# Kernel optimization log

Measured on AMD Instinct MI355X. Metric: run time of the kernel, lower is better.

Reference implementation:

```python
import jax, jax.numpy as jnp
import numpy as np

COMMITMENT_COST = 0.25


def l2norm(x, eps=1e-12):
    # F.normalize along last dim
    n = jnp.linalg.norm(x, axis=-1, keepdims=True)
    return x / jnp.maximum(n, eps)


def vector_quantize(x, codebook, commitment_cost):
    """Euclidean VQ: cdist + argmin, straight-through, VQ loss + perplexity.
    x: (B, N, D), codebook: (K, D)."""
    B, N, D = x.shape
    K = codebook.shape[0]
    flat = x.reshape(-1, D)  # (BN, D)
    # squared euclidean distances via expansion (no (BN,K,D) intermediate)
    d = (jnp.sum(flat * flat, axis=-1, keepdims=True)
         - 2.0 * flat @ codebook.T
         + jnp.sum(codebook * codebook, axis=-1))  # (BN, K)
    idx = jnp.argmin(d, axis=-1)  # (BN,)
    q = codebook[idx]  # (BN, D)
    # VQ losses
    e_latent = jnp.mean((jax.lax.stop_gradient(q) - flat) ** 2)
    q_latent = jnp.mean((q - jax.lax.stop_gradient(flat)) ** 2)
    loss = q_latent + commitment_cost * e_latent
    # perplexity over codebook usage (bincount, not dense one-hot)
    counts = jnp.zeros((K,), flat.dtype).at[idx].add(1.0)
    probs = counts / idx.shape[0]
    perplexity = jnp.exp(-jnp.sum(probs * jnp.log(probs + 1e-10)))
    return idx.reshape(B, N), perplexity, loss


def transform_mfcc(X):
    # wave_embedding.transform_freq: normalize frames, then rfft -> real -> bins 2:40
    Xn = l2norm(X)
    spec = jnp.fft.rfft(Xn, axis=-1).real[..., 2:40]  # (B, N, 38)
    return l2norm(spec)  # mfcc_embedding.norm_fn


def setup_inputs() -> dict:
    key = jax.random.key(0)
    k1, k2, k3 = jax.random.split(key, 3)
    X = jax.random.normal(k1, (16, 4096, 80), dtype=jnp.float32)
    wave_codebook = jax.random.normal(k2, (1024, 80), dtype=jnp.float32)
    mfcc_codebook = jax.random.normal(k3, (256, 38), dtype=jnp.float32)
    return {"X": X, "wave_codebook": wave_codebook, "mfcc_codebook": mfcc_codebook}


def reference(X, wave_codebook, mfcc_codebook):
    K_wave = wave_codebook.shape[0]
    wave_idx, wave_ppl, wave_loss = vector_quantize(X, wave_codebook, COMMITMENT_COST)
    X_mfcc = transform_mfcc(X)
    mfcc_idx, mfcc_ppl, mfcc_loss = vector_quantize(X_mfcc, mfcc_codebook, COMMITMENT_COST)
    mfcc_idx = mfcc_idx + K_wave
    # rearrange stack([wave, mfcc], dim=1): 'b c n -> b (n c)' -> interleave per frame
    B, N = wave_idx.shape
    encodings = jnp.stack([wave_idx, mfcc_idx], axis=-1).reshape(B, 2 * N)
    return encodings, wave_ppl, wave_loss, mfcc_ppl, mfcc_loss
```

## Files before the change

kernel.cpp:

```cpp
#include <hip/hip_runtime.h>
#include <hip/hip_bf16.h>
#include <math.h>


#define NROWS 65536
#define DW    80
#define KW    1024
#define DM    38
#define KM    256
#define CHUNK 128
#define NCHK  8
#define CT_PER 8

typedef __attribute__((ext_vector_type(8))) short bf16x8;
typedef __attribute__((ext_vector_type(4))) float f32x4;

__device__ __forceinline__ void bf16split(float v, short& h, short& l) {
    __hip_bfloat16 hb = __float2bfloat16(v);
    float hf = __bfloat162float(hb);
    __hip_bfloat16 lb = __float2bfloat16(v - hf);
    h = *(short*)&hb;
    l = *(short*)&lb;
}

__device__ __forceinline__ void bf16split3(float v, short& a, short& b, short& c) {
    __hip_bfloat16 h = __float2bfloat16(v);
    float hf = __bfloat162float(h);
    float r = v - hf;
    __hip_bfloat16 m = __float2bfloat16(r);
    float mf = __bfloat162float(m);
    __hip_bfloat16 lo = __float2bfloat16(r - mf);
    a = *(short*)&h; b = *(short*)&m; c = *(short*)&lo;
}

__device__ __forceinline__ bf16x8 bf8zero() {
    bf16x8 z;
    #pragma unroll
    for (int j = 0; j < 8; ++j) z[j] = 0;
    return z;
}

#define WS_SUMS   0
#define WS_HIST   256
#define WS_CNW    5376
#define WS_CNM    9472
#define WS_COSTAB 10496
#define WS_CTF    23296
#define WS_CBF    46336

__global__ __launch_bounds__(256) void prep_kernel(
    const float* __restrict__ cbw, const float* __restrict__ cbm,
    float* __restrict__ sums, int* __restrict__ hist,
    float* __restrict__ cn_w, float* __restrict__ cn_m,
    float* __restrict__ costab)
{
    int idx = blockIdx.x * 256 + threadIdx.x;
    if (idx < KW) {
        const float* p = cbw + (size_t)idx * DW;
        float s = 0.f;
        for (int i = 0; i < DW; ++i) s = fmaf(p[i], p[i], s);
        cn_w[idx] = s;
    } else if (idx < KW + KM) {
        int i = idx - KW;
        const float* p = cbm + (size_t)i * DM;
        float s = 0.f;
        for (int j = 0; j < DM; ++j) s = fmaf(p[j], p[j], s);
        cn_m[i] = s;
    } else if (idx < KW + KM + DW * 40) {
        int t = idx - (KW + KM);
        int d = t / 40, j = t % 40;
        double v = (j < DM)
            ? cos(2.0 * 3.14159265358979323846 * (double)((j + 2) * d) / 80.0)
            : 0.0;
        costab[t] = (float)v;
    } else if (idx == KW + KM + DW * 40)      sums[0] = 0.f;
    else if (idx == KW + KM + DW * 40 + 1)    sums[1] = 0.f;
    else if (idx >= 4482 && idx < 4482 + 1280) hist[idx - 4482] = 0;
}

__global__ __launch_bounds__(256) void prep2_kernel(
    const float* __restrict__ costab, const float* __restrict__ cbm,
    short* __restrict__ ctf, short* __restrict__ cbf)
{
    int idx = blockIdx.x * 256 + threadIdx.x;
    if (idx < 3840) {
        int col, k;
        if (idx < 3072) {
            int j = idx & 7, l = (idx >> 3) & 63, t = idx >> 9;
            col = (t >> 1) * 16 + (l & 15);
            k = 32 * (t & 1) + 8 * (l >> 4) + j;
        } else {
            int i2 = idx - 3072;
            int j = i2 & 7, l = (i2 >> 3) & 31, ct = i2 >> 8;
            col = ct * 16 + (l & 15);
            k = 64 + 8 * (l >> 4) + j;
        }
        float v = (col < 40) ? costab[k * 40 + col] : 0.f;
        short a, b, c; bf16split3(v, a, b, c);
        ctf[idx] = a; ctf[3840 + idx] = b; ctf[7680 + idx] = c;
    } else if (idx < 16128) {
        int i3 = idx - 3840;
        int code, k;
        if (i3 < 8192) {
            int j = i3 & 7, l = (i3 >> 3) & 63, ct = i3 >> 9;
            code = ct * 16 + (l & 15);
            k = 8 * (l >> 4) + j;
        } else {
            int i4 = i3 - 8192;
            int j = i4 & 7, l = (i4 >> 3) & 31, ct = i4 >> 8;
            code = ct * 16 + (l & 15);
            k = 32 + 8 * (l >> 4) + j;
        }
        float v = (k < DM) ? cbm[(size_t)code * DM + k] : 0.f;
        short a, b, c; bf16split3(v, a, b, c);
        cbf[i3] = a; cbf[12288 + i3] = b; cbf[24576 + i3] = c;
    }
}

__global__ __launch_bounds__(256) void wave_vq_mfma(
    const float* __restrict__ X, const float* __restrict__ cb,
    const float* __restrict__ cn, float* __restrict__ out,
    float* __restrict__ sums)
{
    __shared__ short Bh[2][CT_PER * 3 * 64 * 8];
    __shared__ short Bl[2][CT_PER * 3 * 64 * 8];
    __shared__ float cnl[2][CHUNK];
    __shared__ float redw[4];

    const int tid = threadIdx.x;
    const int l   = tid & 63;
    const int qu  = tid >> 6;
    const int c16 = l & 15;
    const int g   = l >> 4;
    const size_t rowbase = (size_t)blockIdx.x * 256 + (size_t)qu * 64;

    bf16x8 Ah[4][3], Al[4][3];
    float xs2[4] = {0.f, 0.f, 0.f, 0.f};
    #pragma unroll
    for (int rt = 0; rt < 4; ++rt) {
        #pragma unroll
        for (int s = 0; s < 3; ++s) {
            const int k0 = 32 * s + 8 * g;
            bf16x8 ah, al;
            if (k0 < DW) {
                const float4* ap =
                    (const float4*)(X + (rowbase + rt * 16 + c16) * DW + k0);
                float4 u = ap[0], w = ap[1];
                float f[8] = {u.x, u.y, u.z, u.w, w.x, w.y, w.z, w.w};
                #pragma unroll
                for (int j = 0; j < 8; ++j) {
                    short hh, ll;
                    bf16split(f[j], hh, ll);
                    ah[j] = hh; al[j] = ll;
                    xs2[rt] = fmaf(f[j], f[j], xs2[rt]);
                }
            } else {
                ah = bf8zero(); al = bf8zero();
            }
            Ah[rt][s] = ah; Al[rt][s] = al;
        }
    }
    #pragma unroll
    for (int rt = 0; rt < 4; ++rt) {
        xs2[rt] += __shfl_xor(xs2[rt], 16, 64);
        xs2[rt] += __shfl_xor(xs2[rt], 32, 64);
    }

    for (int i = tid; i < CT_PER * 32 * 8; i += 256) {
        int ctt = i >> 8;
        int rem = i & 255;
        int lane = 32 + (rem >> 3), j = rem & 7;
        int off = ((ctt * 3 + 2) * 64 + lane) * 8 + j;
        Bh[0][off] = 0; Bh[1][off] = 0; Bl[0][off] = 0; Bl[1][off] = 0;
    }

    auto stage = [&](int c, int b) {
        const float4* src = (const float4*)(cb + (size_t)c * CHUNK * DW);
        #pragma unroll
        for (int i = 0; i < 10; ++i) {
            int q4 = i * 256 + tid;
            float4 v = src[q4];
            int cl = q4 / 20;
            int kb = (q4 - cl * 20) * 4;
            int ctt = cl >> 4, cc = cl & 15;
            int s = kb >> 5, kl = kb & 31, gg = kl >> 3, j0 = kl & 7;
            int off = ((ctt * 3 + s) * 64 + gg * 16 + cc) * 8 + j0;
            short h0, h1, h2, h3, l0, l1, l2, l3;
            bf16split(v.x, h0, l0); bf16split(v.y, h1, l1);
            bf16split(v.z, h2, l2); bf16split(v.w, h3, l3);
            short4 hv = {h0, h1, h2, h3}, lv = {l0, l1, l2, l3};
            *(short4*)&Bh[b][off] = hv;
            *(short4*)&Bl[b][off] = lv;
        }
        if (tid < CHUNK) cnl[b][tid] = cn[c * CHUNK + tid];
    };

    stage(0, 0);
    __syncthreads();

    float bd[4][4];
    int   bi[4][4];
    #pragma unroll
    for (int rt = 0; rt < 4; ++rt)
        #pragma unroll
        for (int i = 0; i < 4; ++i) { bd[rt][i] = 3.4e38f; bi[rt][i] = 0; }

    for (int ch = 0; ch < NCHK; ++ch) {
        const int cur = ch & 1;
        for (int ct = 0; ct < CT_PER; ++ct) {
            const float cnv = cnl[cur][ct * 16 + c16];
            f32x4 acc[4];
            #pragma unroll
            for (int rt = 0; rt < 4; ++rt) acc[rt] = (f32x4){0.f, 0.f, 0.f, 0.f};
            #pragma unroll
            for (int s = 0; s < 3; ++s) {
                const int bo = ((ct * 3 + s) * 64 + l) * 8;
                bf16x8 bh = *(const bf16x8*)&Bh[cur][bo];
                bf16x8 bl = *(const bf16x8*)&Bl[cur][bo];
                #pragma unroll
                for (int rt = 0; rt < 4; ++rt)
                    acc[rt] = __builtin_amdgcn_mfma_f32_16x16x32_bf16(Al[rt][s], bl, acc[rt], 0, 0, 0);
                #pragma unroll
                for (int rt = 0; rt < 4; ++rt)
                    acc[rt] = __builtin_amdgcn_mfma_f32_16x16x32_bf16(Ah[rt][s], bl, acc[rt], 0, 0, 0);
                #pragma unroll
                for (int rt = 0; rt < 4; ++rt)
                    acc[rt] = __builtin_amdgcn_mfma_f32_16x16x32_bf16(Al[rt][s], bh, acc[rt], 0, 0, 0);
                #pragma unroll
                for (int rt = 0; rt < 4; ++rt)
                    acc[rt] = __builtin_amdgcn_mfma_f32_16x16x32_bf16(Ah[rt][s], bh, acc[rt], 0, 0, 0);
            }
            const int idxbase = ch * CHUNK + ct * 16 + c16;
            #pragma unroll
            for (int rt = 0; rt < 4; ++rt) {
                #pragma unroll
                for (int i = 0; i < 4; ++i) {
                    float d = fmaf(-2.f, acc[rt][i], cnv);
                    if (d < bd[rt][i]) { bd[rt][i] = d; bi[rt][i] = idxbase; }
                }
            }
        }
        if (ch + 1 < NCHK) stage(ch + 1, cur ^ 1);
        __syncthreads();
    }

    float lw = 0.f;
    #pragma unroll
    for (int rt = 0; rt < 4; ++rt) {
        #pragma unroll
        for (int i = 0; i < 4; ++i) {
            float d = bd[rt][i]; int ix = bi[rt][i];
            #pragma unroll
            for (int m = 1; m < 16; m <<= 1) {
                float d2 = __shfl_xor(d, m, 64);
                int   i2 = __shfl_xor(ix, m, 64);
                if (d2 < d || (d2 == d && i2 < ix)) { d = d2; ix = i2; }
            }
            float xn = __shfl(xs2[rt], (l & 48) + 4 * (l >> 4) + i, 64);
            if (c16 == 0) {
                size_t row = rowbase + rt * 16 + 4 * g + i;
                out[2 * row] = (float)ix;
                lw += d + xn;
            }
        }
    }
    #pragma unroll
    for (int m = 1; m < 64; m <<= 1) lw += __shfl_xor(lw, m, 64);
    if (l == 0) redw[qu] = lw;
    __syncthreads();
    if (tid == 0) atomicAdd(&sums[0], redw[0] + redw[1] + redw[2] + redw[3]);
}

__global__ __launch_bounds__(256) void mfcc_mfma(
    const float* __restrict__ X, const float* __restrict__ cn_m,
    const short* __restrict__ ctf, const short* __restrict__ cbf,
    float* __restrict__ out, float* __restrict__ sums)
{
    __shared__ __align__(16) short CT2[11520];
    __shared__ __align__(16) short CB2[36864];
    __shared__ float XF[4][64 * 49];
    __shared__ float CN[KM];
    __shared__ float red4[4];

    const int tid = threadIdx.x;
    const int l   = tid & 63;
    const int w   = tid >> 6;
    const int c16 = l & 15;
    const int g   = l >> 4;
    const size_t rowbase = (size_t)blockIdx.x * 256 + (size_t)w * 64;

    {
        const int4* s1 = (const int4*)ctf;
        for (int i = tid; i < 1440; i += 256) ((int4*)CT2)[i] = s1[i];
        const int4* s2 = (const int4*)cbf;
        for (int i = tid; i < 4608; i += 256) ((int4*)CB2)[i] = s2[i];
        if (tid < KM) CN[tid] = cn_m[tid];
    }
    __syncthreads();

    float* xfl = &XF[w][0];

    #pragma unroll 1
    for (int rt = 0; rt < 4; ++rt) {
        bf16x8 A0[3], A1[3], A2[3];
        #pragma unroll
        for (int s = 0; s < 3; ++s) {
            const int k0 = 32 * s + 8 * g;
            if (k0 < DW) {
                const float4* ap =
                    (const float4*)(X + (rowbase + rt * 16 + c16) * DW + k0);
                float4 u = ap[0], v = ap[1];
                float f[8] = {u.x, u.y, u.z, u.w, v.x, v.y, v.z, v.w};
                bf16x8 a0, a1, a2;
                #pragma unroll
                for (int j = 0; j < 8; ++j) {
                    short aa, bb, cc;
                    bf16split3(f[j], aa, bb, cc);
                    a0[j] = aa; a1[j] = bb; a2[j] = cc;
                }
                A0[s] = a0; A1[s] = a1; A2[s] = a2;
            } else {
                A0[s] = bf8zero(); A1[s] = bf8zero(); A2[s] = bf8zero();
            }
        }

        f32x4 acc[3];
        #pragma unroll
        for (int ct = 0; ct < 3; ++ct) acc[ct] = (f32x4){0.f, 0.f, 0.f, 0.f};

        #pragma unroll
        for (int s = 0; s < 3; ++s) {
            #pragma unroll
            for (int ct = 0; ct < 3; ++ct) {
                bf16x8 b0, b1, b2;
                if (s < 2) {
                    const int off = ((ct * 2 + s) * 64 + l) * 8;
                    b0 = *(const bf16x8*)&CT2[off];
                    b1 = *(const bf16x8*)&CT2[3840 + off];
                    b2 = *(const bf16x8*)&CT2[7680 + off];
                } else if (l < 32) {
                    const int off = 3072 + (ct * 32 + l) * 8;
                    b0 = *(const bf16x8*)&CT2[off];
                    b1 = *(const bf16x8*)&CT2[3840 + off];
                    b2 = *(const bf16x8*)&CT2[7680 + off];
                } else {
                    b0 = bf8zero(); b1 = bf8zero(); b2 = bf8zero();
                }
                acc[ct] = __builtin_amdgcn_mfma_f32_16x16x32_bf16(A2[s], b0, acc[ct], 0, 0, 0);
                acc[ct] = __builtin_amdgcn_mfma_f32_16x16x32_bf16(A1[s], b1, acc[ct], 0, 0, 0);
                acc[ct] = __builtin_amdgcn_mfma_f32_16x16x32_bf16(A0[s], b2, acc[ct], 0, 0, 0);
                acc[ct] = __builtin_amdgcn_mfma_f32_16x16x32_bf16(A1[s], b0, acc[ct], 0, 0, 0);
                acc[ct] = __builtin_amdgcn_mfma_f32_16x16x32_bf16(A0[s], b1, acc[ct], 0, 0, 0);
                acc[ct] = __builtin_amdgcn_mfma_f32_16x16x32_bf16(A0[s], b0, acc[ct], 0, 0, 0);
            }
        }

        #pragma unroll
        for (int i = 0; i < 4; ++i) {
            float n2 = acc[0][i] * acc[0][i];
            n2 = fmaf(acc[1][i], acc[1][i], n2);
            n2 = fmaf(acc[2][i], acc[2][i], n2);
            #pragma unroll
            for (int m = 1; m < 16; m <<= 1) n2 += __shfl_xor(n2, m, 64);
            float inv = 1.0f / fmaxf(sqrtf(n2), 1e-12f);
            const int row_l = rt * 16 + 4 * g + i;
            #pragma unroll
            for (int ct = 0; ct < 3; ++ct)
                xfl[row_l * 49 + ct * 16 + c16] = acc[ct][i] * inv;
        }
    }
    __syncthreads();

    bf16x8 X0[4][3], X1[4][3];
    #pragma unroll
    for (int rt = 0; rt < 4; ++rt) {
        const int r0 = rt * 16 + c16;
        {
            const float* p = &xfl[r0 * 49 + 8 * g];
            bf16x8 q0, q1, q2;
            #pragma unroll
            for (int j = 0; j < 8; ++j) {
                short aa, bb, cc;
                bf16split3(p[j], aa, bb, cc);
                q0[j] = aa; q1[j] = bb; q2[j] = cc;
            }
            X0[rt][0] = q0; X0[rt][1] = q1; X0[rt][2] = q2;
        }
        if (g < 2) {
            const float* p = &xfl[r0 * 49 + 32 + 8 * g];
            bf16x8 q0, q1, q2;
            #pragma unroll
            for (int j = 0; j < 8; ++j) {
                short aa, bb, cc;
                bf16split3(p[j], aa, bb, cc);
                q0[j] = aa; q1[j] = bb; q2[j] = cc;
            }
            X1[rt][0] = q0; X1[rt][1] = q1; X1[rt][2] = q2;
        } else {
            X1[rt][0] = bf8zero(); X1[rt][1] = bf8zero(); X1[rt][2] = bf8zero();
        }
    }

    float bd[4][4];
    int   bi[4][4];
    #pragma unroll
    for (int rt = 0; rt < 4; ++rt)
        #pragma unroll
        for (int i = 0; i < 4; ++i) { bd[rt][i] = 3.4e38f; bi[rt][i] = 0; }

    #pragma unroll 1
    for (int ct = 0; ct < 16; ++ct) {
        bf16x8 B0[3], B1[3];
        const int off0 = (ct * 64 + l) * 8;
        B0[0] = *(const bf16x8*)&CB2[off0];
        B0[1] = *(const bf16x8*)&CB2[12288 + off0];
        B0[2] = *(const bf16x8*)&CB2[24576 + off0];
        if (l < 32) {
            const int off1 = 8192 + (ct * 32 + l) * 8;
            B1[0] = *(const bf16x8*)&CB2[off1];
            B1[1] = *(const bf16x8*)&CB2[12288 + off1];
            B1[2] = *(const bf16x8*)&CB2[24576 + off1];
        } else {
            B1[0] = bf8zero(); B1[1] = bf8zero(); B1[2] = bf8zero();
        }
        const float cnv = CN[ct * 16 + c16];
        const int idxbase = ct * 16 + c16;
        #pragma unroll
        for (int rt = 0; rt < 4; ++rt) {
            f32x4 a = (f32x4){0.f, 0.f, 0.f, 0.f};
            a = __builtin_amdgcn_mfma_f32_16x16x32_bf16(X0[rt][2], B0[0], a, 0, 0, 0);
            a = __builtin_amdgcn_mfma_f32_16x16x32_bf16(X0[rt][1], B0[1], a, 0, 0, 0);
            a = __builtin_amdgcn_mfma_f32_16x16x32_bf16(X0[rt][0], B0[2], a, 0, 0, 0);
            a = __builtin_amdgcn_mfma_f32_16x16x32_bf16(X1[rt][2], B1[0], a, 0, 0, 0);
            a = __builtin_amdgcn_mfma_f32_16x16x32_bf16(X1[rt][1], B1[1], a, 0, 0, 0);
            a = __builtin_amdgcn_mfma_f32_16x16x32_bf16(X1[rt][0], B1[2], a, 0, 0, 0);
            a = __builtin_amdgcn_mfma_f32_16x16x32_bf16(X0[rt][1], B0[0], a, 0, 0, 0);
            a = __builtin_amdgcn_mfma_f32_16x16x32_bf16(X0[rt][0], B0[1], a, 0, 0, 0);
            a = __builtin_amdgcn_mfma_f32_16x16x32_bf16(X1[rt][1], B1[0], a, 0, 0, 0);
            a = __builtin_amdgcn_mfma_f32_16x16x32_bf16(X1[rt][0], B1[1], a, 0, 0, 0);
            a = __builtin_amdgcn_mfma_f32_16x16x32_bf16(X0[rt][0], B0[0], a, 0, 0, 0);
            a = __builtin_amdgcn_mfma_f32_16x16x32_bf16(X1[rt][0], B1[0], a, 0, 0, 0);
            #pragma unroll
            for (int i = 0; i < 4; ++i) {
                float d = fmaf(-2.f, a[i], cnv);
                if (d < bd[rt][i]) { bd[rt][i] = d; bi[rt][i] = idxbase; }
            }
        }
    }

    float lm = 0.f;
    #pragma unroll
    for (int rt = 0; rt < 4; ++rt) {
        #pragma unroll
        for (int i = 0; i < 4; ++i) {
            float d = bd[rt][i]; int ix = bi[rt][i];
            #pragma unroll
            for (int m = 1; m < 16; m <<= 1) {
                float d2 = __shfl_xor(d, m, 64);
                int   i2 = __shfl_xor(ix, m, 64);
                if (d2 < d || (d2 == d && i2 < ix)) { d = d2; ix = i2; }
            }
            if (c16 == 0) {
                size_t row = rowbase + rt * 16 + 4 * g + i;
                out[2 * row + 1] = (float)(ix + KW);
                lm += d + 1.0f;
            }
        }
    }
    #pragma unroll
    for (int m = 1; m < 64; m <<= 1) lm += __shfl_xor(lm, m, 64);
    if (l == 0) red4[w] = lm;
    __syncthreads();
    if (tid == 0) atomicAdd(&sums[1], red4[0] + red4[1] + red4[2] + red4[3]);
}

__global__ __launch_bounds__(256) void hist_kernel(
    const float* __restrict__ out, int* __restrict__ hist)
{
    __shared__ int h[1280];
    const int tid = threadIdx.x;
    for (int i = tid; i < 1280; i += 256) h[i] = 0;
    __syncthreads();
    const int base = blockIdx.x * 4096;
    for (int rr = tid; rr < 4096; rr += 256) {
        const int r = base + rr;
        atomicAdd(&h[(int)out[2 * r]], 1);
        atomicAdd(&h[1024 + ((int)out[2 * r + 1] - KW)], 1);
    }
    __syncthreads();
    for (int i = tid; i < 1280; i += 256)
        if (h[i]) atomicAdd(&hist[i], h[i]);
}

__global__ __launch_bounds__(256) void finalize_kernel(
    const int* __restrict__ hist, const float* __restrict__ sums,
    float* __restrict__ out)
{
    __shared__ float red[4];
    const int tid = threadIdx.x;
    const bool wv = (blockIdx.x == 0);
    const int K = wv ? KW : KM;
    const int base = wv ? 0 : 1024;
    float s = 0.f;
    for (int i = tid; i < K; i += 256) {
        float p = (float)hist[base + i] * (1.0f / 65536.0f);
        s += p * logf(p + 1e-10f);
    }
    #pragma unroll
    for (int off = 32; off >= 1; off >>= 1) s += __shfl_xor(s, off, 64);
    if ((tid & 63) == 0) red[tid >> 6] = s;
    __syncthreads();
    if (tid == 0) {
        float t = red[0] + red[1] + red[2] + red[3];
        float ppl = expf(-t);
        float denom = wv ? (float)(NROWS * DW) : (float)(NROWS * DM);
        int obase = 2 * NROWS + (wv ? 0 : 2);
        out[obase]     = ppl;
        out[obase + 1] = 1.25f * sums[wv ? 0 : 1] / denom;
    }
}

extern "C" void kernel_launch(void* const* d_in, const int* in_sizes, int n_in,
                              void* d_out, int out_size, void* d_ws, size_t ws_size,
                              hipStream_t stream) {
    const float* X   = (const float*)d_in[0];
    const float* cbw = (const float*)d_in[1];
    const float* cbm = (const float*)d_in[2];
    float* out = (float*)d_out;

    char* ws = (char*)d_ws;
    float* sums   = (float*)(ws + WS_SUMS);
    int*   hist   = (int*)(ws + WS_HIST);
    float* cn_w   = (float*)(ws + WS_CNW);
    float* cn_m   = (float*)(ws + WS_CNM);
    float* costab = (float*)(ws + WS_COSTAB);
    short* ctf    = (short*)(ws + WS_CTF);
    short* cbf    = (short*)(ws + WS_CBF);

    prep_kernel<<<23, 256, 0, stream>>>(cbw, cbm, sums, hist, cn_w, cn_m, costab);
    prep2_kernel<<<63, 256, 0, stream>>>(costab, cbm, ctf, cbf);
    wave_vq_mfma<<<NROWS / 256, 256, 0, stream>>>(X, cbw, cn_w, out, sums);
    mfcc_mfma<<<NROWS / 256, 256, 0, stream>>>(X, cn_m, ctf, cbf, out, sums);
    hist_kernel<<<16, 256, 0, stream>>>(out, hist);
    finalize_kernel<<<2, 256, 0, stream>>>(hist, sums, out);
}
```

Baseline: 107.0 us.

## Pre-split wave codebook once and stream MFMA operands from global instead of LDS

The two prep kernels are merged into one that also converts the wave codebook into MFMA-ready bf16 hi/lo fragments once, instead of every block redoing the split and LDS staging. The wave kernel now reads those fragments straight from global memory with a one-tile register prefetch, removing LDS buffers and __syncthreads. The mfcc kernel likewise reads its cos and codebook fragments from global rather than copying them into LDS. Both kernels get launch_bounds occupancy hints, and the histogram uses more blocks. The trade-off is that each block now relies on L2/L1 cache hits for codebook data that was previously held in shared memory.

```diff
diff --git a/kernel.cpp b/kernel.cpp
--- a/kernel.cpp
+++ b/kernel.cpp
@@ -8,9 +8,6 @@
 #define KW    1024
 #define DM    38
 #define KM    256
-#define CHUNK 128
-#define NCHK  8
-#define CT_PER 8
 
 typedef __attribute__((ext_vector_type(8))) short bf16x8;
 typedef __attribute__((ext_vector_type(4))) float f32x4;
@@ -44,62 +41,58 @@
 #define WS_HIST   256
 #define WS_CNW    5376
 #define WS_CNM    9472
-#define WS_COSTAB 10496
-#define WS_CTF    23296
-#define WS_CBF    46336
+#define WS_CTF    10496
+#define WS_CBF    33536
+#define WS_CWH    107264
+#define WS_CWL    303872
 
 __global__ __launch_bounds__(256) void prep_kernel(
     const float* __restrict__ cbw, const float* __restrict__ cbm,
     float* __restrict__ sums, int* __restrict__ hist,
     float* __restrict__ cn_w, float* __restrict__ cn_m,
-    float* __restrict__ costab)
+    short* __restrict__ ctf, short* __restrict__ cbf,
+    short* __restrict__ cwh, short* __restrict__ cwl)
 {
     int idx = blockIdx.x * 256 + threadIdx.x;
-    if (idx < KW) {
-        const float* p = cbw + (size_t)idx * DW;
-        float s = 0.f;
-        for (int i = 0; i < DW; ++i) s = fmaf(p[i], p[i], s);
-        cn_w[idx] = s;
-    } else if (idx < KW + KM) {
-        int i = idx - KW;
-        const float* p = cbm + (size_t)i * DM;
-        float s = 0.f;
-        for (int j = 0; j < DM; ++j) s = fmaf(p[j], p[j], s);
-        cn_m[i] = s;
-    } else if (idx < KW + KM + DW * 40) {
-        int t = idx - (KW + KM);
-        int d = t / 40, j = t % 40;
-        double v = (j < DM)
-            ? cos(2.0 * 3.14159265358979323846 * (double)((j + 2) * d) / 80.0)
-            : 0.0;
-        costab[t] = (float)v;
-    } else if (idx == KW + KM + DW * 40)      sums[0] = 0.f;
-    else if (idx == KW + KM + DW * 40 + 1)    sums[1] = 0.f;
-    else if (idx >= 4482 && idx < 4482 + 1280) hist[idx - 4482] = 0;
-}
-
-__global__ __launch_bounds__(256) void prep2_kernel(
-    const float* __restrict__ costab, const float* __restrict__ cbm,
-    short* __restrict__ ctf, short* __restrict__ cbf)
-{
-    int idx = blockIdx.x * 256 + threadIdx.x;
-    if (idx < 3840) {
+    if (idx < 12288) {
+        const int f = idx;
+        const int ct = f / 192, rem = f % 192, s = rem >> 6, l = rem & 63;
+        const int code = ct * 16 + (l & 15);
+        const int k0 = 32 * s + 8 * (l >> 4);
+        bf16x8 h, lo;
+        if (k0 < DW) {
+            const float4* p = (const float4*)(cbw + (size_t)code * DW + k0);
+            float4 u = p[0], v = p[1];
+            float fv[8] = {u.x, u.y, u.z, u.w, v.x, v.y, v.z, v.w};
+            #pragma unroll
+            for (int j = 0; j < 8; ++j) {
+                short hh, ll;
+                bf16split(fv[j], hh, ll);
+                h[j] = hh; lo[j] = ll;
+            }
+        } else { h = bf8zero(); lo = bf8zero(); }
+        *(bf16x8*)&cwh[(size_t)f * 8] = h;
+        *(bf16x8*)&cwl[(size_t)f * 8] = lo;
+    } else if (idx < 16128) {
+        int t = idx - 12288;
         int col, k;
-        if (idx < 3072) {
-            int j = idx & 7, l = (idx >> 3) & 63, t = idx >> 9;
-            col = (t >> 1) * 16 + (l & 15);
-            k = 32 * (t & 1) + 8 * (l >> 4) + j;
+        if (t < 3072) {
+            int j = t & 7, l = (t >> 3) & 63, tt = t >> 9;
+            col = (tt >> 1) * 16 + (l & 15);
+            k = 32 * (tt & 1) + 8 * (l >> 4) + j;
         } else {
-            int i2 = idx - 3072;
+            int i2 = t - 3072;
             int j = i2 & 7, l = (i2 >> 3) & 31, ct = i2 >> 8;
             col = ct * 16 + (l & 15);
             k = 64 + 8 * (l >> 4) + j;
         }
-        float v = (col < 40) ? costab[k * 40 + col] : 0.f;
+        float v = (col < DM)
+            ? (float)cos(2.0 * 3.14159265358979323846 * (double)((col + 2) * k) / 80.0)
+            : 0.f;
         short a, b, c; bf16split3(v, a, b, c);
-        ctf[idx] = a; ctf[3840 + idx] = b; ctf[7680 + idx] = c;
-    } else if (idx < 16128) {
-        int i3 = idx - 3840;
+        ctf[t] = a; ctf[3840 + t] = b; ctf[7680 + t] = c;
+    } else if (idx < 28416) {
+        int i3 = idx - 16128;
         int code, k;
         if (i3 < 8192) {
             int j = i3 & 7, l = (i3 >> 3) & 63, ct = i3 >> 9;
@@ -114,17 +107,29 @@
         float v = (k < DM) ? cbm[(size_t)code * DM + k] : 0.f;
         short a, b, c; bf16split3(v, a, b, c);
         cbf[i3] = a; cbf[12288 + i3] = b; cbf[24576 + i3] = c;
-    }
-}
-
-__global__ __launch_bounds__(256) void wave_vq_mfma(
-    const float* __restrict__ X, const float* __restrict__ cb,
-    const float* __restrict__ cn, float* __restrict__ out,
-    float* __restrict__ sums)
+    } else if (idx < 29440) {
+        int i = idx - 28416;
+        const float* p = cbw + (size_t)i * DW;
+        float s = 0.f;
+        for (int k = 0; k < DW; ++k) s = fmaf(p[k], p[k], s);
+        cn_w[i] = s;
+    } else if (idx < 29696) {
+        int i = idx - 29440;
+        const float* p = cbm + (size_t)i * DM;
+        float s = 0.f;
+        for (int j = 0; j < DM; ++j) s = fmaf(p[j], p[j], s);
+        cn_m[i] = s;
+    } else if (idx < 30976) {
+        hist[idx - 29696] = 0;
+    } else if (idx == 30976) sums[0] = 0.f;
+    else if (idx == 30977)   sums[1] = 0.f;
+}
+
+__global__ __launch_bounds__(256, 2) void wave_vq_mfma(
+    const float* __restrict__ X, const short* __restrict__ cwh,
+    const short* __restrict__ cwl, const float* __restrict__ cn,
+    float* __restrict__ out, float* __restrict__ sums)
 {
-    __shared__ short Bh[2][CT_PER * 3 * 64 * 8];
-    __shared__ short Bl[2][CT_PER * 3 * 64 * 8];
-    __shared__ float cnl[2][CHUNK];
     __shared__ float redw[4];
 
     const int tid = threadIdx.x;
@@ -166,38 +171,6 @@
         xs2[rt] += __shfl_xor(xs2[rt], 32, 64);
     }
 
-    for (int i = tid; i < CT_PER * 32 * 8; i += 256) {
-        int ctt = i >> 8;
-        int rem = i & 255;
-        int lane = 32 + (rem >> 3), j = rem & 7;
-        int off = ((ctt * 3 + 2) * 64 + lane) * 8 + j;
-        Bh[0][off] = 0; Bh[1][off] = 0; Bl[0][off] = 0; Bl[1][off] = 0;
-    }
-
-    auto stage = [&](int c, int b) {
-        const float4* src = (const float4*)(cb + (size_t)c * CHUNK * DW);
-        #pragma unroll
-        for (int i = 0; i < 10; ++i) {
-            int q4 = i * 256 + tid;
-            float4 v = src[q4];
-            int cl = q4 / 20;
-            int kb = (q4 - cl * 20) * 4;
-            int ctt = cl >> 4, cc = cl & 15;
-            int s = kb >> 5, kl = kb & 31, gg = kl >> 3, j0 = kl & 7;
-            int off = ((ctt * 3 + s) * 64 + gg * 16 + cc) * 8 + j0;
-            short h0, h1, h2, h3, l0, l1, l2, l3;
-            bf16split(v.x, h0, l0); bf16split(v.y, h1, l1);
-            bf16split(v.z, h2, l2); bf16split(v.w, h3, l3);
-            short4 hv = {h0, h1, h2, h3}, lv = {l0, l1, l2, l3};
-            *(short4*)&Bh[b][off] = hv;
-            *(short4*)&Bl[b][off] = lv;
-        }
-        if (tid < CHUNK) cnl[b][tid] = cn[c * CHUNK + tid];
-    };
-
-    stage(0, 0);
-    __syncthreads();
-
     float bd[4][4];
     int   bi[4][4];
     #pragma unroll
@@ -205,43 +178,59 @@
         #pragma unroll
         for (int i = 0; i < 4; ++i) { bd[rt][i] = 3.4e38f; bi[rt][i] = 0; }
 
-    for (int ch = 0; ch < NCHK; ++ch) {
-        const int cur = ch & 1;
-        for (int ct = 0; ct < CT_PER; ++ct) {
-            const float cnv = cnl[cur][ct * 16 + c16];
-            f32x4 acc[4];
-            #pragma unroll
-            for (int rt = 0; rt < 4; ++rt) acc[rt] = (f32x4){0.f, 0.f, 0.f, 0.f};
+    const bf16x8* Hsrc = (const bf16x8*)cwh;
+    const bf16x8* Lsrc = (const bf16x8*)cwl;
+
+    bf16x8 pbh[3], pbl[3];
+    #pragma unroll
+    for (int s = 0; s < 3; ++s) {
+        pbh[s] = Hsrc[s * 64 + l];
+        pbl[s] = Lsrc[s * 64 + l];
+    }
+    float pcn = cn[c16];
+
+    #pragma unroll 1
+    for (int ct = 0; ct < 64; ++ct) {
+        bf16x8 bh[3], bl[3];
+        #pragma unroll
+        for (int s = 0; s < 3; ++s) { bh[s] = pbh[s]; bl[s] = pbl[s]; }
+        const float cnv = pcn;
+        if (ct < 63) {
             #pragma unroll
             for (int s = 0; s < 3; ++s) {
-                const int bo = ((ct * 3 + s) * 64 + l) * 8;
-                bf16x8 bh = *(const bf16x8*)&Bh[cur][bo];
-                bf16x8 bl = *(const bf16x8*)&Bl[cur][bo];
-                #pragma unroll
-                for (int rt = 0; rt < 4; ++rt)
-                    acc[rt] = __builtin_amdgcn_mfma_f32_16x16x32_bf16(Al[rt][s], bl, acc[rt], 0, 0, 0);
-                #pragma unroll
-                for (int rt = 0; rt < 4; ++rt)
-                    acc[rt] = __builtin_amdgcn_mfma_f32_16x16x32_bf16(Ah[rt][s], bl, acc[rt], 0, 0, 0);
-                #pragma unroll
-                for (int rt = 0; rt < 4; ++rt)
-                    acc[rt] = __builtin_amdgcn_mfma_f32_16x16x32_bf16(Al[rt][s], bh, acc[rt], 0, 0, 0);
-                #pragma unroll
-                for (int rt = 0; rt < 4; ++rt)
-                    acc[rt] = __builtin_amdgcn_mfma_f32_16x16x32_bf16(Ah[rt][s], bh, acc[rt], 0, 0, 0);
-            }
-            const int idxbase = ch * CHUNK + ct * 16 + c16;
-            #pragma unroll
-            for (int rt = 0; rt < 4; ++rt) {
-                #pragma unroll
-                for (int i = 0; i < 4; ++i) {
-                    float d = fmaf(-2.f, acc[rt][i], cnv);
-                    if (d < bd[rt][i]) { bd[rt][i] = d; bi[rt][i] = idxbase; }
-                }
-            }
-        }
-        if (ch + 1 < NCHK) stage(ch + 1, cur ^ 1);
-        __syncthreads();
+                pbh[s] = Hsrc[((ct + 1) * 3 + s) * 64 + l];
+                pbl[s] = Lsrc[((ct + 1) * 3 + s) * 64 + l];
+            }
+            pcn = cn[(ct + 1) * 16 + c16];
+        }
+
+        f32x4 acc[4];
+        #pragma unroll
+        for (int rt = 0; rt < 4; ++rt) acc[rt] = (f32x4){0.f, 0.f, 0.f, 0.f};
+        #pragma unroll
+        for (int s = 0; s < 3; ++s) {
+            #pragma unroll
+            for (int rt = 0; rt < 4; ++rt)
+                acc[rt] = __builtin_amdgcn_mfma_f32_16x16x32_bf16(Al[rt][s], bl[s], acc[rt], 0, 0, 0);
+            #pragma unroll
+            for (int rt = 0; rt < 4; ++rt)
+                acc[rt] = __builtin_amdgcn_mfma_f32_16x16x32_bf16(Ah[rt][s], bl[s], acc[rt], 0, 0, 0);
+            #pragma unroll
+            for (int rt = 0; rt < 4; ++rt)
+                acc[rt] = __builtin_amdgcn_mfma_f32_16x16x32_bf16(Al[rt][s], bh[s], acc[rt], 0, 0, 0);
+            #pragma unroll
+            for (int rt = 0; rt < 4; ++rt)
+                acc[rt] = __builtin_amdgcn_mfma_f32_16x16x32_bf16(Ah[rt][s], bh[s], acc[rt], 0, 0, 0);
+        }
+        const int idxbase = ct * 16 + c16;
+        #pragma unroll
+        for (int rt = 0; rt < 4; ++rt) {
+            #pragma unroll
+            for (int i = 0; i < 4; ++i) {
+                float d = fmaf(-2.f, acc[rt][i], cnv);
+                if (d < bd[rt][i]) { bd[rt][i] = d; bi[rt][i] = idxbase; }
+            }
+        }
     }
 
     float lw = 0.f;
@@ -271,13 +260,11 @@
     if (tid == 0) atomicAdd(&sums[0], redw[0] + redw[1] + redw[2] + redw[3]);
 }
 
-__global__ __launch_bounds__(256) void mfcc_mfma(
+__global__ __launch_bounds__(256, 2) void mfcc_mfma(
     const float* __restrict__ X, const float* __restrict__ cn_m,
     const short* __restrict__ ctf, const short* __restrict__ cbf,
     float* __restrict__ out, float* __restrict__ sums)
 {
-    __shared__ __align__(16) short CT2[11520];
-    __shared__ __align__(16) short CB2[36864];
     __shared__ float XF[4][64 * 49];
     __shared__ float CN[KM];
     __shared__ float red4[4];
@@ -289,13 +276,7 @@
     const int g   = l >> 4;
     const size_t rowbase = (size_t)blockIdx.x * 256 + (size_t)w * 64;
 
-    {
-        const int4* s1 = (const int4*)ctf;
-        for (int i = tid; i < 1440; i += 256) ((int4*)CT2)[i] = s1[i];
-        const int4* s2 = (const int4*)cbf;
-        for (int i = tid; i < 4608; i += 256) ((int4*)CB2)[i] = s2[i];
-        if (tid < KM) CN[tid] = cn_m[tid];
-    }
+    if (tid < KM) CN[tid] = cn_m[tid];
     __syncthreads();
 
     float* xfl = &XF[w][0];
@@ -335,14 +316,14 @@
                 bf16x8 b0, b1, b2;
                 if (s < 2) {
                     const int off = ((ct * 2 + s) * 64 + l) * 8;
-                    b0 = *(const bf16x8*)&CT2[off];
-                    b1 = *(const bf16x8*)&CT2[3840 + off];
-                    b2 = *(const bf16x8*)&CT2[7680 + off];
+                    b0 = *(const bf16x8*)&ctf[off];
+                    b1 = *(const bf16x8*)&ctf[3840 + off];
+                    b2 = *(const bf16x8*)&ctf[7680 + off];
                 } else if (l < 32) {
                     const int off = 3072 + (ct * 32 + l) * 8;
-                    b0 = *(const bf16x8*)&CT2[off];
-                    b1 = *(const bf16x8*)&CT2[3840 + off];
-                    b2 = *(const bf16x8*)&CT2[7680 + off];
+                    b0 = *(const bf16x8*)&ctf[off];
+                    b1 = *(const bf16x8*)&ctf[3840 + off];
+                    b2 = *(const bf16x8*)&ctf[7680 + off];
                 } else {
                     b0 = bf8zero(); b1 = bf8zero(); b2 = bf8zero();
                 }
@@ -412,14 +393,14 @@
     for (int ct = 0; ct < 16; ++ct) {
         bf16x8 B0[3], B1[3];
         const int off0 = (ct * 64 + l) * 8;
-        B0[0] = *(const bf16x8*)&CB2[off0];
-        B0[1] = *(const bf16x8*)&CB2[12288 + off0];
-        B0[2] = *(const bf16x8*)&CB2[24576 + off0];
+        B0[0] = *(const bf16x8*)&cbf[off0];
+        B0[1] = *(const bf16x8*)&cbf[12288 + off0];
+        B0[2] = *(const bf16x8*)&cbf[24576 + off0];
         if (l < 32) {
             const int off1 = 8192 + (ct * 32 + l) * 8;
-            B1[0] = *(const bf16x8*)&CB2[off1];
-            B1[1] = *(const bf16x8*)&CB2[12288 + off1];
-            B1[2] = *(const bf16x8*)&CB2[24576 + off1];
+            B1[0] = *(const bf16x8*)&cbf[off1];
+            B1[1] = *(const bf16x8*)&cbf[12288 + off1];
+            B1[2] = *(const bf16x8*)&cbf[24576 + off1];
         } else {
             B1[0] = bf8zero(); B1[1] = bf8zero(); B1[2] = bf8zero();
         }
@@ -481,8 +462,8 @@
     const int tid = threadIdx.x;
     for (int i = tid; i < 1280; i += 256) h[i] = 0;
     __syncthreads();
-    const int base = blockIdx.x * 4096;
-    for (int rr = tid; rr < 4096; rr += 256) {
+    const int base = blockIdx.x * 1024;
+    for (int rr = tid; rr < 1024; rr += 256) {
         const int r = base + rr;
         atomicAdd(&h[(int)out[2 * r]], 1);
         atomicAdd(&h[1024 + ((int)out[2 * r + 1] - KW)], 1);
@@ -529,18 +510,19 @@
     float* out = (float*)d_out;
 
     char* ws = (char*)d_ws;
-    float* sums   = (float*)(ws + WS_SUMS);
-    int*   hist   = (int*)(ws + WS_HIST);
-    float* cn_w   = (float*)(ws + WS_CNW);
-    float* cn_m   = (float*)(ws + WS_CNM);
-    float* costab = (float*)(ws + WS_COSTAB);
-    short* ctf    = (short*)(ws + WS_CTF);
-    short* cbf    = (short*)(ws + WS_CBF);
-
-    prep_kernel<<<23, 256, 0, stream>>>(cbw, cbm, sums, hist, cn_w, cn_m, costab);
-    prep2_kernel<<<63, 256, 0, stream>>>(costab, cbm, ctf, cbf);
-    wave_vq_mfma<<<NROWS / 256, 256, 0, stream>>>(X, cbw, cn_w, out, sums);
+    float* sums = (float*)(ws + WS_SUMS);
+    int*   hist = (int*)(ws + WS_HIST);
+    float* cn_w = (float*)(ws + WS_CNW);
+    float* cn_m = (float*)(ws + WS_CNM);
+    short* ctf  = (short*)(ws + WS_CTF);
+    short* cbf  = (short*)(ws + WS_CBF);
+    short* cwh  = (short*)(ws + WS_CWH);
+    short* cwl  = (short*)(ws + WS_CWL);
+
+    prep_kernel<<<122, 256, 0, stream>>>(cbw, cbm, sums, hist, cn_w, cn_m,
+                                         ctf, cbf, cwh, cwl);
+    wave_vq_mfma<<<NROWS / 256, 256, 0, stream>>>(X, cwh, cwl, cn_w, out, sums);
     mfcc_mfma<<<NROWS / 256, 256, 0, stream>>>(X, cn_m, ctf, cbf, out, sums);
-    hist_kernel<<<16, 256, 0, stream>>>(out, hist);
+    hist_kernel<<<64, 256, 0, stream>>>(out, hist);
     finalize_kernel<<<2, 256, 0, stream>>>(hist, sums, out);
 }
```

Measured after the change: 94.13 us. -12.0%, faster.
